# Performance work log

Measured on AMD Instinct MI355X. Metric: run time of the kernel, lower is better.

The kernel has to match this reference:

```python
import jax, jax.numpy as jnp
import numpy as np

RADIUS = 0.1
NSAMPLE = 32
EPS = 1e-5


def ball_query(p, radius, k):
    # p: (B,N,3) -> idx: (B,N,k) int32. For each query point, take the first k
    # points (in index order) within `radius`; pad with the first found index.
    B, N, _ = p.shape
    d2 = jnp.sum((p[:, :, None, :] - p[:, None, :, :]) ** 2, axis=-1)  # (B,N,N)
    j = jnp.arange(N, dtype=jnp.int32)
    key = jnp.where(d2 < radius * radius, j[None, None, :], N)  # invalid -> N
    neg_small, _ = jax.lax.top_k(-key, k)  # k smallest keys, ascending
    idx = -neg_small                        # (B,N,k)
    first = idx[..., :1]
    idx = jnp.where(idx == N, first, idx)   # pad missing neighbors with first
    return idx


def conv_bn_relu(f, W, g, b, relu=True):
    # f: (B,Cin,N,K); W: (Cout,Cin) 1x1 conv; BatchNorm2d (training stats) + ReLU
    y = jnp.einsum('oc,bcnk->bonk', W, f)
    mean = jnp.mean(y, axis=(0, 2, 3), keepdims=True)
    var = jnp.var(y, axis=(0, 2, 3), keepdims=True)
    y = (y - mean) * jax.lax.rsqrt(var + EPS)
    y = y * g[None, :, None, None] + b[None, :, None, None]
    return jax.nn.relu(y) if relu else y


def reference(p, x, W1, g1, b1, W2, g2, b2):
    # p: (B,N,3), x: (B,C,N)
    B, N, _ = p.shape
    idx = ball_query(p, RADIUS, NSAMPLE)                    # (B,N,K)
    pj = jax.vmap(lambda pts, ix: pts[ix])(p, idx)          # (B,N,K,3)
    dp = pj - p[:, :, None, :]                              # relative coords
    dp = jnp.transpose(dp, (0, 3, 1, 2))                    # (B,3,N,K)
    xt = jnp.transpose(x, (0, 2, 1))                        # (B,N,C)
    xj = jax.vmap(lambda ft, ix: ft[ix])(xt, idx)           # (B,N,K,C)
    xj = jnp.transpose(xj, (0, 3, 1, 2))                    # (B,C,N,K)
    f = jnp.concatenate([dp, xj], axis=1)                   # (B,3+C,N,K)
    f = conv_bn_relu(f, W1, g1, b1, relu=True)
    f = conv_bn_relu(f, W2, g2, b2, relu=True)              # last_act=True
    return jnp.max(f, axis=-1)                              # (B,Cout,N)


def setup_inputs() -> dict:
    key = jax.random.key(0)
    ks = jax.random.split(key, 4)
    B, N, C = 4, 4096, 32
    Cin, Cout = 3 + C, 64
    return {
        'p': jax.random.uniform(ks[0], (B, N, 3), dtype=jnp.float32),
        'x': jax.random.normal(ks[1], (B, C, N), dtype=jnp.float32),
        'W1': jax.random.normal(ks[2], (Cout, Cin), dtype=jnp.float32) * 0.1,
        'g1': jnp.ones((Cout,), jnp.float32),
        'b1': jnp.zeros((Cout,), jnp.float32),
        'W2': jax.random.normal(ks[3], (Cout, Cout), dtype=jnp.float32) * 0.1,
        'g2': jnp.ones((Cout,), jnp.float32),
        'b2': jnp.zeros((Cout,), jnp.float32),
    }
```

## Files before the change

### kernel.cpp

```cpp
#include <hip/hip_runtime.h>
#include <stdint.h>


#define R2 0.01f
#define INVM (1.0f / 524288.0f)

typedef __bf16 bf16x8 __attribute__((ext_vector_type(8)));
typedef float f32x4 __attribute__((ext_vector_type(4)));

__device__ __forceinline__ uint32_t pack_bf16(float a, float b) {
  uint32_t ua = __float_as_uint(a), ub = __float_as_uint(b);
  ua += 0x7fffu + ((ua >> 16) & 1u);
  ub += 0x7fffu + ((ub >> 16) & 1u);
  return (ua >> 16) | (ub & 0xffff0000u);
}
__device__ __forceinline__ float bf_lo(uint32_t v) { return __uint_as_float(v << 16); }
__device__ __forceinline__ float bf_hi(uint32_t v) { return __uint_as_float(v & 0xffff0000u); }

__device__ __forceinline__ int cell_of(float v) {
  const int c = (int)(v * 10.f);
  return c > 9 ? 9 : c;
}

__global__ __launch_bounds__(1024) void k_front(const float* __restrict__ p,
                                                const float* __restrict__ x,
                                                const float* __restrict__ W1,
                                                const float* __restrict__ W2,
                                                void* __restrict__ u,
                                                float* __restrict__ q,
                                                uint32_t* __restrict__ w2frag,
                                                float* __restrict__ part1b,
                                                float* __restrict__ part2b,
                                                float4* __restrict__ cellpts,
                                                int* __restrict__ cellStart) {
  __shared__ __align__(16) char smraw[61440];
  const int bid = blockIdx.x, tid = threadIdx.x;

  if (bid < 128) {
    float* W1s = (float*)smraw;
    for (int tt = tid; tt < 2240; tt += 1024) {
      const int o = tt / 35, cc = tt - o * 35;
      W1s[(cc << 6) + o] = W1[tt];
    }
    __syncthreads();
    const int t = tid & 255, sb = tid >> 8;
    const int g = (bid << 7) + (sb << 5) + (t & 31);
    const int b = g >> 12, nl = g & 4095;
    const int os = (t >> 5) << 3;
    float f[35];
    const float* pb = p + g * 3;
    f[0] = pb[0]; f[1] = pb[1]; f[2] = pb[2];
    const float* xb = x + (b << 17) + nl;
#pragma unroll
    for (int cc = 0; cc < 32; ++cc) f[3 + cc] = xb[cc << 12];
    float acc[8];
#pragma unroll
    for (int o = 0; o < 8; ++o) acc[o] = 0.f;
#pragma unroll
    for (int cc = 0; cc < 35; ++cc) {
      const float fc = f[cc];
      const float4* wp = (const float4*)(W1s + (cc << 6) + os);
      const float4 w0 = wp[0], w1 = wp[1];
      acc[0] = fmaf(w0.x, fc, acc[0]); acc[1] = fmaf(w0.y, fc, acc[1]);
      acc[2] = fmaf(w0.z, fc, acc[2]); acc[3] = fmaf(w0.w, fc, acc[3]);
      acc[4] = fmaf(w1.x, fc, acc[4]); acc[5] = fmaf(w1.y, fc, acc[5]);
      acc[6] = fmaf(w1.z, fc, acc[6]); acc[7] = fmaf(w1.w, fc, acc[7]);
      if (cc == 2) {
        *(float4*)(q + (g << 6) + os)     = make_float4(acc[0], acc[1], acc[2], acc[3]);
        *(float4*)(q + (g << 6) + os + 4) = make_float4(acc[4], acc[5], acc[6], acc[7]);
      }
    }
    uint4 pk;
    pk.x = pack_bf16(acc[0], acc[1]);
    pk.y = pack_bf16(acc[2], acc[3]);
    pk.z = pack_bf16(acc[4], acc[5]);
    pk.w = pack_bf16(acc[6], acc[7]);
    *(uint4*)((char*)u + ((size_t)g << 7) + (os << 1)) = pk;
    return;
  }

  if (bid == 128) {
    for (int tt = tid; tt < 2048; tt += 1024) {
      const int e2 = tt & 3, lane = (tt >> 2) & 63, frag = tt >> 8;
      const int kt = frag >> 2, ot = frag & 3;
      const int c0 = kt * 32 + ((lane >> 4) << 3) + e2 * 2;
      const int o = ot * 16 + (lane & 15);
      w2frag[tt] = pack_bf16(W2[(o << 6) + c0], W2[(o << 6) + c0 + 1]);
    }
    part1b[tid] = 0.f;
    part2b[tid] = 0.f;
    return;
  }

  float* px = (float*)smraw;
  float* py = px + 4096;
  float* pz = py + 4096;
  int* cnt_s = (int*)(smraw + 49152);
  int* scanA = (int*)(smraw + 53248);
  int* scanB = (int*)(smraw + 57344);
  const int b = bid - 129;
  const float* pb = p + b * 12288;
  cnt_s[tid] = 0;
  for (int i = tid; i < 4096; i += 1024) {
    px[i] = pb[3 * i]; py[i] = pb[3 * i + 1]; pz[i] = pb[3 * i + 2];
  }
  __syncthreads();
  for (int i = tid; i < 4096; i += 1024) {
    const int c = (cell_of(px[i]) * 10 + cell_of(py[i])) * 10 + cell_of(pz[i]);
    atomicAdd(&cnt_s[c], 1);
  }
  __syncthreads();
  int* src = scanA; int* dst = scanB;
  src[tid] = cnt_s[tid];
  __syncthreads();
  for (int d = 1; d < 1024; d <<= 1) {
    int v = src[tid];
    if (tid >= d) v += src[tid - d];
    dst[tid] = v;
    __syncthreads();
    int* tmp = src; src = dst; dst = tmp;
  }
  const int excl = (tid == 0) ? 0 : src[tid - 1];
  if (tid <= 1000) cellStart[b * 1001 + tid] = (tid < 1000) ? excl : src[999];
  cnt_s[tid] = excl;
  __syncthreads();
  for (int i = tid; i < 4096; i += 1024) {
    const float xx = px[i], yy = py[i], zz = pz[i];
    const int c = (cell_of(xx) * 10 + cell_of(yy)) * 10 + cell_of(zz);
    const int pos = atomicAdd(&cnt_s[c], 1);
    cellpts[(b << 12) + pos] = make_float4(xx, yy, zz, __int_as_float(i));
  }
}

__global__ __launch_bounds__(256) void k_query(const float* __restrict__ p,
                                               const float4* __restrict__ cellpts,
                                               const int* __restrict__ cellStart,
                                               int* __restrict__ idx) {
  __shared__ uint32_t bm[4][128];
  const int tid = threadIdx.x, w = tid >> 6, lane = tid & 63;
  const int blk0 = blockIdx.x;
  const int blkS = ((blk0 & 7) << 9) + (blk0 >> 3);
  const int n = (blkS << 2) + w;
  const int b = n >> 12;
  bm[w][lane] = 0; bm[w][64 + lane] = 0;
  const float qx = p[n * 3], qy = p[n * 3 + 1], qz = p[n * 3 + 2];
  const int cxq = cell_of(qx), cyq = cell_of(qy), czq = cell_of(qz);

  int cnt_l = 0, startG = 0;
  if (lane < 9) {
    const int cx = cxq + lane / 3 - 1;
    const int cy = cyq + lane % 3 - 1;
    if ((unsigned)cx < 10u && (unsigned)cy < 10u) {
      const int zlo = czq > 0 ? czq - 1 : 0;
      const int zhi = czq < 9 ? czq + 1 : 9;
      const int* cs = cellStart + b * 1001 + (cx * 10 + cy) * 10;
      startG = cs[zlo];
      cnt_l = cs[zhi + 1] - startG;
    }
  }
  int incl = cnt_l;
#pragma unroll
  for (int d = 1; d < 64; d <<= 1) { const int t = __shfl_up(incl, d); if (lane >= d) incl += t; }
  const int T = __shfl(incl, 63);
  const int base_l = startG - (incl - cnt_l);

  for (int tb = 0; tb < T; tb += 64) {
    const int t = tb + lane;
    int s = 0;
#pragma unroll
    for (int m = 0; m < 9; ++m) s += (__shfl(incl, m) <= t);
    const int a = __shfl(base_l, s < 9 ? s : 8);
    if (t < T) {
      const float4 cp = cellpts[(b << 12) + a + t];
      const float dx = cp.x - qx, dy = cp.y - qy, dz = cp.z - qz;
      const float d2 = __fadd_rn(__fadd_rn(__fmul_rn(dx, dx), __fmul_rn(dy, dy)),
                                 __fmul_rn(dz, dz));
      if (d2 < R2) {
        const int j = __float_as_int(cp.w);
        atomicOr(&bm[w][j >> 5], 1u << (j & 31));
      }
    }
  }
  __threadfence_block();

  const uint2 wp2 = *(const uint2*)&bm[w][2 * lane];
  unsigned long long wd = ((unsigned long long)wp2.y << 32) | wp2.x;
  const int pc = __popcll(wd);
  int ip = pc;
#pragma unroll
  for (int d = 1; d < 64; d <<= 1) { const int t = __shfl_up(ip, d); if (lane >= d) ip += t; }
  const int cntT = __shfl(ip, 63);
  int bpos = ip - pc;
  const unsigned long long nz = __ballot(wd != 0ull);
  const int fl = (int)__builtin_ctzll(nz);
  const int fv = wd ? ((lane << 6) + (int)__builtin_ctzll(wd)) : 0;
  const int first = __shfl(fv, fl);
  int* row = idx + (n << 5);
  unsigned long long ww = wd;
  while (ww && bpos < 32) {
    const int j = (lane << 6) + (int)__builtin_ctzll(ww);
    row[bpos] = j;
    ++bpos;
    ww &= ww - 1;
  }
  for (int s = cntT + lane; s < 32; s += 64) row[s] = first;
}

__global__ __launch_bounds__(256) void k_bn1(const void* __restrict__ u,
                                             const float* __restrict__ q,
                                             const int* __restrict__ idx,
                                             float* __restrict__ part1b) {
  __shared__ int idxs[512];
  __shared__ __align__(16) float qs[1024];
  __shared__ float red[8][64];
  const int tid = threadIdx.x;
  const int blk0 = blockIdx.x;
  const int blkS = ((blk0 & 7) << 7) + (blk0 >> 3);
  const int p0 = blkS << 4;
  const int bb = (p0 >> 12) << 12;
  idxs[tid] = idx[(p0 << 5) + tid];
  idxs[256 + tid] = idx[(p0 << 5) + 256 + tid];
#pragma unroll
  for (int i = 0; i < 4; ++i) qs[(i << 8) + tid] = q[(p0 << 6) + (i << 8) + tid];
  __syncthreads();
  const int c4 = tid & 3;
  const char* ub = (const char*)u;
  float s1[16], s2[16];
#pragma unroll
  for (int i = 0; i < 16; ++i) { s1[i] = 0.f; s2[i] = 0.f; }
#pragma unroll 2
  for (int pass = 0; pass < 8; ++pass) {
    const int r = (pass << 6) + (tid >> 2);
    const int j = idxs[r];
    const int pt = r >> 5;
    const uint4* up = (const uint4*)(ub + ((size_t)(bb + j) << 7) + (c4 << 5));
    const uint4 u0 = up[0], u1 = up[1];
    const float* qp = qs + (pt << 6) + (c4 << 4);
    const uint32_t uw[8] = {u0.x, u0.y, u0.z, u0.w, u1.x, u1.y, u1.z, u1.w};
#pragma unroll
    for (int e = 0; e < 8; ++e) {
      const float y0 = bf_lo(uw[e]) - qp[2 * e];
      const float y1 = bf_hi(uw[e]) - qp[2 * e + 1];
      s1[2 * e] += y0;     s2[2 * e] = fmaf(y0, y0, s2[2 * e]);
      s1[2 * e + 1] += y1; s2[2 * e + 1] = fmaf(y1, y1, s2[2 * e + 1]);
    }
  }
#pragma unroll
  for (int i = 0; i < 16; ++i) {
#pragma unroll
    for (int d = 4; d <= 32; d <<= 1) {
      s1[i] += __shfl_xor(s1[i], d);
      s2[i] += __shfl_xor(s2[i], d);
    }
  }
  const int w = tid >> 6, l = tid & 63;
  if (l < 4) {
#pragma unroll
    for (int i = 0; i < 16; ++i) {
      const int ch = (l << 4) + i;
      red[(w << 1)][ch] = s1[i];
      red[(w << 1) + 1][ch] = s2[i];
    }
  }
  __syncthreads();
  if (tid < 128) {
    const int ch = tid & 63, stat = tid >> 6;
    const float v = red[stat][ch] + red[2 + stat][ch] + red[4 + stat][ch] + red[6 + stat][ch];
    atomicAdd(&part1b[((blk0 & 7) << 7) + (stat << 6) + ch], v);
  }
}

__global__ __launch_bounds__(256) void k_stage2(const void* __restrict__ u,
                                                const int* __restrict__ idx,
                                                const float* __restrict__ q,
                                                const float* __restrict__ part1b,
                                                const float* __restrict__ g1,
                                                const float* __restrict__ b1,
                                                const uint32_t* __restrict__ w2frag,
                                                float* __restrict__ part2b,
                                                uint32_t* __restrict__ ymm) {
  __shared__ uint32_t hl[8192];
  __shared__ float rs[8][64];
  __shared__ int   idxs[256];
  __shared__ float ac[128];
  __shared__ float red[8][64];
  const int tid = threadIdx.x, w = tid >> 6, l = tid & 63;
  const int blk0 = blockIdx.x;
  const int blk = ((blk0 & 7) << 8) + (blk0 >> 3);
  const int p0 = blk << 3;
  const int bb = (p0 >> 12) << 12;

  idxs[tid] = idx[(p0 << 5) + tid];
  const float qa = q[(p0 << 6) + tid];
  const float qb = q[(p0 << 6) + 256 + tid];
  if (tid < 64) {
    float s1 = 0.f, s2 = 0.f;
#pragma unroll
    for (int xx = 0; xx < 8; ++xx) {
      s1 += part1b[(xx << 7) + tid];
      s2 += part1b[(xx << 7) + 64 + tid];
    }
    const float mean = s1 * INVM, var = s2 * INVM - mean * mean;
    const float a = g1[tid] * rsqrtf(var + 1e-5f);
    ac[tid] = a; ac[64 + tid] = b1[tid] - mean * a;
  }
  __syncthreads();
  rs[tid >> 6][tid & 63] = fmaf(-ac[tid & 63], qa, ac[64 + (tid & 63)]);
  rs[4 + (tid >> 6)][tid & 63] = fmaf(-ac[tid & 63], qb, ac[64 + (tid & 63)]);
  __syncthreads();

  const int c = tid & 3;
  const char* ub = (const char*)u;
  f32x4 av[4];
#pragma unroll
  for (int k = 0; k < 4; ++k) av[k] = *(const f32x4*)&ac[(c << 4) + (k << 2)];
#pragma unroll
  for (int pass = 0; pass < 4; ++pass) {
    const int r = (pass << 6) + (tid >> 2);
    const int pt = r >> 5;
    const int j = idxs[r];
    const uint4* up = (const uint4*)(ub + ((size_t)(bb + j) << 7) + (c << 5));
    const uint4 u0 = up[0], u1 = up[1];
    f32x4 rv4[4];
#pragma unroll
    for (int k = 0; k < 4; ++k) rv4[k] = *(const f32x4*)&rs[pt][(c << 4) + (k << 2)];
    const uint32_t uw8[8] = {u0.x, u0.y, u0.z, u0.w, u1.x, u1.y, u1.z, u1.w};
    uint32_t pk[8];
#pragma unroll
    for (int e = 0; e < 8; ++e) {
      const int i0 = 2 * e, i1 = 2 * e + 1;
      const float h0 = fmaxf(fmaf(av[i0 >> 2][i0 & 3], bf_lo(uw8[e]), rv4[i0 >> 2][i0 & 3]), 0.f);
      const float h1 = fmaxf(fmaf(av[i1 >> 2][i1 & 3], bf_hi(uw8[e]), rv4[i1 >> 2][i1 & 3]), 0.f);
      pk[e] = pack_bf16(h0, h1);
    }
    const int byte0 = (r << 7) + (c << 5);
    const int sw = (r & 7) << 4;
    *(uint4*)((char*)hl + (byte0 ^ sw)) = make_uint4(pk[0], pk[1], pk[2], pk[3]);
    *(uint4*)((char*)hl + ((byte0 + 16) ^ sw)) = make_uint4(pk[4], pk[5], pk[6], pk[7]);
  }

  bf16x8 bfr[8];
#pragma unroll
  for (int f = 0; f < 8; ++f)
    bfr[f] = __builtin_bit_cast(bf16x8, *(const uint4*)&w2frag[(f << 8) + (l << 2)]);
  __syncthreads();

  float sm_[4] = {0.f, 0.f, 0.f, 0.f}, sq[4] = {0.f, 0.f, 0.f, 0.f};
#pragma unroll 1
  for (int pi = 0; pi < 2; ++pi) {
    const int ptl = (w << 1) + pi;
    const int pn = p0 + ptl;
    float mx[4], mn[4];
#pragma unroll
    for (int ot = 0; ot < 4; ++ot) { mx[ot] = -3e38f; mn[ot] = 3e38f; }
#pragma unroll
    for (int kt2 = 0; kt2 < 2; ++kt2) {
      bf16x8 afr[2];
#pragma unroll
      for (int kt = 0; kt < 2; ++kt) {
        const int srow = (ptl << 5) + (kt2 << 4) + (l & 15);
        int byte = (srow << 7) + (kt << 6) + ((l >> 4) << 4);
        byte ^= (srow & 7) << 4;
        afr[kt] = *(const bf16x8*)((const char*)hl + byte);
      }
#pragma unroll
      for (int ot = 0; ot < 4; ++ot) {
        f32x4 acc = {0.f, 0.f, 0.f, 0.f};
        acc = __builtin_amdgcn_mfma_f32_16x16x32_bf16(afr[0], bfr[ot], acc, 0, 0, 0);
        acc = __builtin_amdgcn_mfma_f32_16x16x32_bf16(afr[1], bfr[4 + ot], acc, 0, 0, 0);
#pragma unroll
        for (int e = 0; e < 4; ++e) {
          const float v = acc[e];
          mx[ot] = fmaxf(mx[ot], v); mn[ot] = fminf(mn[ot], v);
          sm_[ot] += v; sq[ot] = fmaf(v, v, sq[ot]);
        }
      }
    }
#pragma unroll
    for (int ot = 0; ot < 4; ++ot) {
      float a = fmaxf(mx[ot], __shfl_xor(mx[ot], 16)); a = fmaxf(a, __shfl_xor(a, 32));
      float b = fminf(mn[ot], __shfl_xor(mn[ot], 16)); b = fminf(b, __shfl_xor(b, 32));
      const int o = (ot << 4) + (l & 15);
      if (l < 16) ymm[(pn << 6) + o] = pack_bf16(a, b);
    }
  }
#pragma unroll
  for (int ot = 0; ot < 4; ++ot) {
    float s = sm_[ot]; s += __shfl_xor(s, 16); s += __shfl_xor(s, 32);
    float t2 = sq[ot]; t2 += __shfl_xor(t2, 16); t2 += __shfl_xor(t2, 32);
    if (l < 16) { red[w][(ot << 4) + l] = s; red[4 + w][(ot << 4) + l] = t2; }
  }
  __syncthreads();
  if (tid < 128) {
    const int ch = tid & 63, sel = (tid >= 64) ? 4 : 0;
    const float v = red[sel][ch] + red[sel + 1][ch] + red[sel + 2][ch] + red[sel + 3][ch];
    atomicAdd(&part2b[((blk0 & 7) << 7) + tid], v);
  }
}

__global__ __launch_bounds__(256) void k_out(const uint32_t* __restrict__ ymm,
                                             const float* __restrict__ part2b,
                                             const float* __restrict__ g2,
                                             const float* __restrict__ b2,
                                             float* __restrict__ out) {
  __shared__ float ac[128];
  __shared__ float tile[64][65];
  const int tid = threadIdx.x;
  if (tid < 64) {
    float s1 = 0.f, s2 = 0.f;
#pragma unroll
    for (int xx = 0; xx < 8; ++xx) {
      s1 += part2b[(xx << 7) + tid];
      s2 += part2b[(xx << 7) + 64 + tid];
    }
    const float mean = s1 * INVM, var = s2 * INVM - mean * mean;
    const float a = g2[tid] * rsqrtf(var + 1e-5f);
    ac[tid] = a; ac[64 + tid] = b2[tid] - mean * a;
  }
  __syncthreads();
  const int b = blockIdx.x >> 6, nt = blockIdx.x & 63;
  const int pnbase = (b << 12) + (nt << 6);
#pragma unroll
  for (int i = 0; i < 16; ++i) {
    const int e = i * 256 + tid;
    const int nl = e >> 6, o = e & 63;
    const float a = ac[o], c = ac[64 + o];
    const uint32_t v = ymm[((pnbase + nl) << 6) + o];
    const float val = (a >= 0.f) ? bf_lo(v) : bf_hi(v);
    tile[nl][o] = fmaxf(fmaf(a, val, c), 0.f);
  }
  __syncthreads();
#pragma unroll
  for (int i = 0; i < 16; ++i) {
    const int e = i * 256 + tid;
    const int ol = e >> 6, nl = e & 63;
    out[(b << 18) + (ol << 12) + (nt << 6) + nl] = tile[nl][ol];
  }
}

extern "C" void kernel_launch(void* const* d_in, const int* in_sizes, int n_in,
                              void* d_out, int out_size, void* d_ws, size_t ws_size,
                              hipStream_t stream) {
  const float* p  = (const float*)d_in[0];
  const float* x  = (const float*)d_in[1];
  const float* W1 = (const float*)d_in[2];
  const float* g1 = (const float*)d_in[3];
  const float* b1 = (const float*)d_in[4];
  const float* W2 = (const float*)d_in[5];
  const float* g2 = (const float*)d_in[6];
  const float* b2 = (const float*)d_in[7];
  float* out = (float*)d_out;

  char* ws = (char*)d_ws;
  size_t off = 0;
  int* idx        = (int*)(ws + off);      off += 2097152;
  void* u         = (void*)(ws + off);     off += 2097152;
  float* q        = (float*)(ws + off);    off += 4194304;
  uint32_t* w2f   = (uint32_t*)(ws + off); off += 8192;
  float* part1b   = (float*)(ws + off);    off += 4096;
  float* part2b   = (float*)(ws + off);    off += 4096;
  uint32_t* ymm   = (uint32_t*)(ws + off); off += 2097152;
  float4* cellpts = (float4*)(ws + off);   off += 262144;
  int* cellStart  = (int*)(ws + off);      off += 16384;

  k_front<<<dim3(133), dim3(1024), 0, stream>>>(p, x, W1, W2, u, q, w2f,
                                                part1b, part2b, cellpts, cellStart);
  k_query<<<dim3(4096), dim3(256), 0, stream>>>(p, cellpts, cellStart, idx);
  k_bn1<<<dim3(1024), dim3(256), 0, stream>>>(u, q, idx, part1b);
  k_stage2<<<dim3(2048), dim3(256), 0, stream>>>(u, idx, q, part1b, g1, b1, w2f,
                                                 part2b, ymm);
  k_out<<<dim3(256), dim3(256), 0, stream>>>(ymm, part2b, g2, b2, out);
}
```

Before: 54.78 us.

## Build MFMA A-fragments directly in registers from gathered rows, drop LDS staging

The stage-2 kernel no longer stages BN1+ReLU activations in a 32KB shared buffer. Each lane now gathers the neighbour rows it needs straight from global memory, applies the scale/shift and ReLU in registers, and packs the MFMA A fragments directly. This removes the LDS write/read round trip and one barrier, and cuts LDS use, which may allow more resident blocks. In exchange, each lane issues smaller 16-byte gathers with a less coalesced access pattern, and register pressure goes up.

```diff
diff --git a/kernel.cpp b/kernel.cpp
--- a/kernel.cpp
+++ b/kernel.cpp
@@ -279,7 +279,6 @@
                                                 const uint32_t* __restrict__ w2frag,
                                                 float* __restrict__ part2b,
                                                 uint32_t* __restrict__ ymm) {
-  __shared__ uint32_t hl[8192];
   __shared__ float rs[8][64];
   __shared__ int   idxs[256];
   __shared__ float ac[128];
@@ -307,67 +306,73 @@
   __syncthreads();
   rs[tid >> 6][tid & 63] = fmaf(-ac[tid & 63], qa, ac[64 + (tid & 63)]);
   rs[4 + (tid >> 6)][tid & 63] = fmaf(-ac[tid & 63], qb, ac[64 + (tid & 63)]);
-  __syncthreads();
-
-  const int c = tid & 3;
-  const char* ub = (const char*)u;
-  f32x4 av[4];
-#pragma unroll
-  for (int k = 0; k < 4; ++k) av[k] = *(const f32x4*)&ac[(c << 4) + (k << 2)];
-#pragma unroll
-  for (int pass = 0; pass < 4; ++pass) {
-    const int r = (pass << 6) + (tid >> 2);
-    const int pt = r >> 5;
-    const int j = idxs[r];
-    const uint4* up = (const uint4*)(ub + ((size_t)(bb + j) << 7) + (c << 5));
-    const uint4 u0 = up[0], u1 = up[1];
-    f32x4 rv4[4];
-#pragma unroll
-    for (int k = 0; k < 4; ++k) rv4[k] = *(const f32x4*)&rs[pt][(c << 4) + (k << 2)];
-    const uint32_t uw8[8] = {u0.x, u0.y, u0.z, u0.w, u1.x, u1.y, u1.z, u1.w};
-    uint32_t pk[8];
-#pragma unroll
-    for (int e = 0; e < 8; ++e) {
-      const int i0 = 2 * e, i1 = 2 * e + 1;
-      const float h0 = fmaxf(fmaf(av[i0 >> 2][i0 & 3], bf_lo(uw8[e]), rv4[i0 >> 2][i0 & 3]), 0.f);
-      const float h1 = fmaxf(fmaf(av[i1 >> 2][i1 & 3], bf_hi(uw8[e]), rv4[i1 >> 2][i1 & 3]), 0.f);
-      pk[e] = pack_bf16(h0, h1);
-    }
-    const int byte0 = (r << 7) + (c << 5);
-    const int sw = (r & 7) << 4;
-    *(uint4*)((char*)hl + (byte0 ^ sw)) = make_uint4(pk[0], pk[1], pk[2], pk[3]);
-    *(uint4*)((char*)hl + ((byte0 + 16) ^ sw)) = make_uint4(pk[4], pk[5], pk[6], pk[7]);
-  }
 
   bf16x8 bfr[8];
 #pragma unroll
   for (int f = 0; f < 8; ++f)
     bfr[f] = __builtin_bit_cast(bf16x8, *(const uint4*)&w2frag[(f << 8) + (l << 2)]);
   __syncthreads();
+
+  const char* ub = (const char*)u;
+  const int cg = l >> 4;
+  f32x4 av[2][2];
+#pragma unroll
+  for (int kt = 0; kt < 2; ++kt) {
+    av[kt][0] = *(const f32x4*)&ac[(kt << 5) + (cg << 3)];
+    av[kt][1] = *(const f32x4*)&ac[(kt << 5) + (cg << 3) + 4];
+  }
 
   float sm_[4] = {0.f, 0.f, 0.f, 0.f}, sq[4] = {0.f, 0.f, 0.f, 0.f};
 #pragma unroll 1
   for (int pi = 0; pi < 2; ++pi) {
     const int ptl = (w << 1) + pi;
     const int pn = p0 + ptl;
+    const int j0 = idxs[(ptl << 5) + (l & 15)];
+    const int j1 = idxs[(ptl << 5) + 16 + (l & 15)];
+    const char* r0 = ub + ((size_t)(bb + j0) << 7) + (cg << 4);
+    const char* r1 = ub + ((size_t)(bb + j1) << 7) + (cg << 4);
+    uint4 raw[2][2];
+    raw[0][0] = *(const uint4*)(r0);
+    raw[0][1] = *(const uint4*)(r0 + 64);
+    raw[1][0] = *(const uint4*)(r1);
+    raw[1][1] = *(const uint4*)(r1 + 64);
+    f32x4 rv[2][2];
+#pragma unroll
+    for (int kt = 0; kt < 2; ++kt) {
+      rv[kt][0] = *(const f32x4*)&rs[ptl][(kt << 5) + (cg << 3)];
+      rv[kt][1] = *(const f32x4*)&rs[ptl][(kt << 5) + (cg << 3) + 4];
+    }
+    bf16x8 afr[2][2];
+#pragma unroll
+    for (int kt2 = 0; kt2 < 2; ++kt2) {
+#pragma unroll
+      for (int kt = 0; kt < 2; ++kt) {
+        const uint4 rw = raw[kt2][kt];
+        const uint32_t uw4[4] = {rw.x, rw.y, rw.z, rw.w};
+        uint4 pk;
+        uint32_t* pkp = (uint32_t*)&pk;
+#pragma unroll
+        for (int e2 = 0; e2 < 4; ++e2) {
+          const int i0 = 2 * e2, i1 = 2 * e2 + 1;
+          const float h0 = fmaxf(fmaf(av[kt][i0 >> 2][i0 & 3], bf_lo(uw4[e2]),
+                                      rv[kt][i0 >> 2][i0 & 3]), 0.f);
+          const float h1 = fmaxf(fmaf(av[kt][i1 >> 2][i1 & 3], bf_hi(uw4[e2]),
+                                      rv[kt][i1 >> 2][i1 & 3]), 0.f);
+          pkp[e2] = pack_bf16(h0, h1);
+        }
+        afr[kt2][kt] = __builtin_bit_cast(bf16x8, pk);
+      }
+    }
     float mx[4], mn[4];
 #pragma unroll
     for (int ot = 0; ot < 4; ++ot) { mx[ot] = -3e38f; mn[ot] = 3e38f; }
 #pragma unroll
     for (int kt2 = 0; kt2 < 2; ++kt2) {
-      bf16x8 afr[2];
-#pragma unroll
-      for (int kt = 0; kt < 2; ++kt) {
-        const int srow = (ptl << 5) + (kt2 << 4) + (l & 15);
-        int byte = (srow << 7) + (kt << 6) + ((l >> 4) << 4);
-        byte ^= (srow & 7) << 4;
-        afr[kt] = *(const bf16x8*)((const char*)hl + byte);
-      }
 #pragma unroll
       for (int ot = 0; ot < 4; ++ot) {
         f32x4 acc = {0.f, 0.f, 0.f, 0.f};
-        acc = __builtin_amdgcn_mfma_f32_16x16x32_bf16(afr[0], bfr[ot], acc, 0, 0, 0);
-        acc = __builtin_amdgcn_mfma_f32_16x16x32_bf16(afr[1], bfr[4 + ot], acc, 0, 0, 0);
+        acc = __builtin_amdgcn_mfma_f32_16x16x32_bf16(afr[kt2][0], bfr[ot], acc, 0, 0, 0);
+        acc = __builtin_amdgcn_mfma_f32_16x16x32_bf16(afr[kt2][1], bfr[4 + ot], acc, 0, 0, 0);
 #pragma unroll
         for (int e = 0; e < 4; ++e) {
           const float v = acc[e];
```

Result: slower. 57.49 us (+4.9%).

## Shrink front blocks, use wave-shuffle cell scan, stage query rows in LDS

Applied to the files above, without the earlier changes.

k_front now runs 512-thread blocks with a much smaller shared buffer. The conv1 work is split over 256 blocks instead of 128. The cell-binning blocks replace the 10-step LDS Hillis-Steele scan with a wave shuffle scan plus per-wave sums. Points are read directly from global memory instead of being staged in shared memory. The W2 fragment and partial-zeroing work moves to the last block. k_query writes each neighbor row into LDS first and then stores it with one coalesced 32-lane write, replacing scattered per-lane global stores. The intent is better occupancy and shorter critical-path binning, at the cost of reading p twice from global memory.

```diff
diff --git a/kernel.cpp b/kernel.cpp
--- a/kernel.cpp
+++ b/kernel.cpp
@@ -22,29 +22,29 @@
   return c > 9 ? 9 : c;
 }
 
-__global__ __launch_bounds__(1024) void k_front(const float* __restrict__ p,
-                                                const float* __restrict__ x,
-                                                const float* __restrict__ W1,
-                                                const float* __restrict__ W2,
-                                                void* __restrict__ u,
-                                                float* __restrict__ q,
-                                                uint32_t* __restrict__ w2frag,
-                                                float* __restrict__ part1b,
-                                                float* __restrict__ part2b,
-                                                float4* __restrict__ cellpts,
-                                                int* __restrict__ cellStart) {
-  __shared__ __align__(16) char smraw[61440];
+__global__ __launch_bounds__(512) void k_front(const float* __restrict__ p,
+                                               const float* __restrict__ x,
+                                               const float* __restrict__ W1,
+                                               const float* __restrict__ W2,
+                                               void* __restrict__ u,
+                                               float* __restrict__ q,
+                                               uint32_t* __restrict__ w2frag,
+                                               float* __restrict__ part1b,
+                                               float* __restrict__ part2b,
+                                               float4* __restrict__ cellpts,
+                                               int* __restrict__ cellStart) {
+  __shared__ __align__(16) char smraw[8960];
   const int bid = blockIdx.x, tid = threadIdx.x;
 
-  if (bid < 128) {
+  if (bid < 256) {
     float* W1s = (float*)smraw;
-    for (int tt = tid; tt < 2240; tt += 1024) {
+    for (int tt = tid; tt < 2240; tt += 512) {
       const int o = tt / 35, cc = tt - o * 35;
       W1s[(cc << 6) + o] = W1[tt];
     }
     __syncthreads();
     const int t = tid & 255, sb = tid >> 8;
-    const int g = (bid << 7) + (sb << 5) + (t & 31);
+    const int g = (bid << 6) + (sb << 5) + (t & 31);
     const int b = g >> 12, nl = g & 4095;
     const int os = (t >> 5) << 3;
     float f[35];
@@ -79,57 +79,55 @@
     return;
   }
 
-  if (bid == 128) {
-    for (int tt = tid; tt < 2048; tt += 1024) {
-      const int e2 = tt & 3, lane = (tt >> 2) & 63, frag = tt >> 8;
-      const int kt = frag >> 2, ot = frag & 3;
-      const int c0 = kt * 32 + ((lane >> 4) << 3) + e2 * 2;
-      const int o = ot * 16 + (lane & 15);
-      w2frag[tt] = pack_bf16(W2[(o << 6) + c0], W2[(o << 6) + c0 + 1]);
-    }
-    part1b[tid] = 0.f;
-    part2b[tid] = 0.f;
+  if (bid < 260) {
+    int* cnt_s = (int*)smraw;
+    int* wsum  = (int*)(smraw + 4096);
+    const int b = bid - 256;
+    const float* pb = p + b * 12288;
+    for (int i = tid; i < 1024; i += 512) cnt_s[i] = 0;
+    __syncthreads();
+    for (int i = tid; i < 4096; i += 512) {
+      const float xx = pb[3 * i], yy = pb[3 * i + 1], zz = pb[3 * i + 2];
+      const int c = (cell_of(xx) * 10 + cell_of(yy)) * 10 + cell_of(zz);
+      atomicAdd(&cnt_s[c], 1);
+    }
+    __syncthreads();
+    const int c0 = cnt_s[2 * tid], c1 = cnt_s[2 * tid + 1];
+    const int chunk = c0 + c1;
+    int incl = chunk;
+#pragma unroll
+    for (int d = 1; d < 64; d <<= 1) {
+      const int t = __shfl_up(incl, d);
+      if ((tid & 63) >= d) incl += t;
+    }
+    const int w = tid >> 6, lane = tid & 63;
+    if (lane == 63) wsum[w] = incl;
+    __syncthreads();
+    int wpre = 0;
+    for (int i = 0; i < w; ++i) wpre += wsum[i];
+    const int excl = wpre + incl - chunk;
+    if (2 * tid <= 1000)     cellStart[b * 1001 + 2 * tid]     = excl;
+    if (2 * tid + 1 <= 1000) cellStart[b * 1001 + 2 * tid + 1] = excl + c0;
+    cnt_s[2 * tid] = excl;
+    cnt_s[2 * tid + 1] = excl + c0;
+    __syncthreads();
+    for (int i = tid; i < 4096; i += 512) {
+      const float xx = pb[3 * i], yy = pb[3 * i + 1], zz = pb[3 * i + 2];
+      const int c = (cell_of(xx) * 10 + cell_of(yy)) * 10 + cell_of(zz);
+      const int pos = atomicAdd(&cnt_s[c], 1);
+      cellpts[(b << 12) + pos] = make_float4(xx, yy, zz, __int_as_float(i));
+    }
     return;
   }
 
-  float* px = (float*)smraw;
-  float* py = px + 4096;
-  float* pz = py + 4096;
-  int* cnt_s = (int*)(smraw + 49152);
-  int* scanA = (int*)(smraw + 53248);
-  int* scanB = (int*)(smraw + 57344);
-  const int b = bid - 129;
-  const float* pb = p + b * 12288;
-  cnt_s[tid] = 0;
-  for (int i = tid; i < 4096; i += 1024) {
-    px[i] = pb[3 * i]; py[i] = pb[3 * i + 1]; pz[i] = pb[3 * i + 2];
-  }
-  __syncthreads();
-  for (int i = tid; i < 4096; i += 1024) {
-    const int c = (cell_of(px[i]) * 10 + cell_of(py[i])) * 10 + cell_of(pz[i]);
-    atomicAdd(&cnt_s[c], 1);
-  }
-  __syncthreads();
-  int* src = scanA; int* dst = scanB;
-  src[tid] = cnt_s[tid];
-  __syncthreads();
-  for (int d = 1; d < 1024; d <<= 1) {
-    int v = src[tid];
-    if (tid >= d) v += src[tid - d];
-    dst[tid] = v;
-    __syncthreads();
-    int* tmp = src; src = dst; dst = tmp;
-  }
-  const int excl = (tid == 0) ? 0 : src[tid - 1];
-  if (tid <= 1000) cellStart[b * 1001 + tid] = (tid < 1000) ? excl : src[999];
-  cnt_s[tid] = excl;
-  __syncthreads();
-  for (int i = tid; i < 4096; i += 1024) {
-    const float xx = px[i], yy = py[i], zz = pz[i];
-    const int c = (cell_of(xx) * 10 + cell_of(yy)) * 10 + cell_of(zz);
-    const int pos = atomicAdd(&cnt_s[c], 1);
-    cellpts[(b << 12) + pos] = make_float4(xx, yy, zz, __int_as_float(i));
-  }
+  for (int tt = tid; tt < 2048; tt += 512) {
+    const int e2 = tt & 3, lane = (tt >> 2) & 63, frag = tt >> 8;
+    const int kt = frag >> 2, ot = frag & 3;
+    const int c0 = kt * 32 + ((lane >> 4) << 3) + e2 * 2;
+    const int o = ot * 16 + (lane & 15);
+    w2frag[tt] = pack_bf16(W2[(o << 6) + c0], W2[(o << 6) + c0 + 1]);
+  }
+  for (int i = tid; i < 1024; i += 512) { part1b[i] = 0.f; part2b[i] = 0.f; }
 }
 
 __global__ __launch_bounds__(256) void k_query(const float* __restrict__ p,
@@ -137,6 +135,7 @@
                                                const int* __restrict__ cellStart,
                                                int* __restrict__ idx) {
   __shared__ uint32_t bm[4][128];
+  __shared__ int rowbuf[4][32];
   const int tid = threadIdx.x, w = tid >> 6, lane = tid & 63;
   const int blk0 = blockIdx.x;
   const int blkS = ((blk0 & 7) << 9) + (blk0 >> 3);
@@ -195,15 +194,16 @@
   const int fl = (int)__builtin_ctzll(nz);
   const int fv = wd ? ((lane << 6) + (int)__builtin_ctzll(wd)) : 0;
   const int first = __shfl(fv, fl);
-  int* row = idx + (n << 5);
   unsigned long long ww = wd;
   while (ww && bpos < 32) {
     const int j = (lane << 6) + (int)__builtin_ctzll(ww);
-    row[bpos] = j;
+    rowbuf[w][bpos] = j;
     ++bpos;
     ww &= ww - 1;
   }
-  for (int s = cntT + lane; s < 32; s += 64) row[s] = first;
+  for (int s = cntT + lane; s < 32; s += 64) rowbuf[w][s] = first;
+  __threadfence_block();
+  if (lane < 32) idx[(n << 5) + lane] = rowbuf[w][lane];
 }
 
 __global__ __launch_bounds__(256) void k_bn1(const void* __restrict__ u,
@@ -463,8 +463,8 @@
   float4* cellpts = (float4*)(ws + off);   off += 262144;
   int* cellStart  = (int*)(ws + off);      off += 16384;
 
-  k_front<<<dim3(133), dim3(1024), 0, stream>>>(p, x, W1, W2, u, q, w2f,
-                                                part1b, part2b, cellpts, cellStart);
+  k_front<<<dim3(261), dim3(512), 0, stream>>>(p, x, W1, W2, u, q, w2f,
+                                               part1b, part2b, cellpts, cellStart);
   k_query<<<dim3(4096), dim3(256), 0, stream>>>(p, cellpts, cellStart, idx);
   k_bn1<<<dim3(1024), dim3(256), 0, stream>>>(u, q, idx, part1b);
   k_stage2<<<dim3(2048), dim3(256), 0, stream>>>(u, idx, q, part1b, g1, b1, w2f,
```

New measurement: 55.12 us. About the same (+0.6%).
